# Kernel tuning notes

Hardware: AMD Instinct MI355X
Metric: run time of the kernel (lower is better)

Reference implementation:

```python
import jax, jax.numpy as jnp
import numpy as np

EPS = 1e-5
RES = [12000, 9000, 6000, 4000]
CH = [9, 64, 128, 256]
SKIPS = 3
FC_N = 128


def batchnorm(x, g, b):
    # train-mode BatchNorm2d over (batch, face) dims; x: [B, C, F]
    m = x.mean(axis=(0, 2), keepdims=True)
    v = x.var(axis=(0, 2), keepdims=True)
    xn = (x - m) * jax.lax.rsqrt(v + EPS)
    return xn * g[None, :, None] + b[None, :, None]


def mesh_conv(x, nbr, w):
    # x: [B, C, F]; nbr: [F, 3] neighbor face ids; w: [O, C, 4]
    n = x[:, :, nbr]                      # [B, C, F, 3] irregular gather
    n1, n2, n3 = n[..., 0], n[..., 1], n[..., 2]
    G = jnp.stack([
        x,
        n1 + n2 + n3,
        jnp.abs(n1 - n2) + jnp.abs(n2 - n3) + jnp.abs(n3 - n1),
        jnp.maximum(jnp.maximum(n1, n2), n3),
    ], axis=-1)                           # [B, C, F, 4] symmetric features
    return jnp.einsum('ocj,bcfj->bof', w, G)


def mres_conv(x, nbr, wc, ws, bng, bnb):
    # MResConvFace: conv0 -> skips x (bn(relu) -> conv) -> +skip -> relu
    x = mesh_conv(x, nbr, wc)
    x1 = x
    for i in range(SKIPS):
        x = batchnorm(jax.nn.relu(x), bng[i], bnb[i])
        x = mesh_conv(x, nbr, ws[i])
    return jax.nn.relu(x + x1)


def setup_inputs() -> dict:
    key = jax.random.key(0)
    ks = jax.random.split(key, 64)
    it = iter(range(64))
    d = {}
    d['x'] = jax.random.normal(ks[next(it)], (8, CH[0], RES[0]), dtype=jnp.float32)
    for i in range(3):
        d[f'nbr{i}'] = jax.random.randint(ks[next(it)], (RES[i], 3), 0, RES[i], dtype=jnp.int32)
        d[f'pool{i}'] = jax.random.randint(ks[next(it)], (RES[i + 1], 3), 0, RES[i], dtype=jnp.int32)
    for i in range(3):
        cin, cout = CH[i], CH[i + 1]
        d[f'wc{i}'] = jax.random.normal(ks[next(it)], (cout, cin, 4), dtype=jnp.float32) * (1.0 / np.sqrt(4 * cin))
        d[f'ws{i}'] = jax.random.normal(ks[next(it)], (SKIPS, cout, cout, 4), dtype=jnp.float32) * (1.0 / np.sqrt(4 * cout))
        d[f'bng{i}'] = jnp.ones((SKIPS, cout), dtype=jnp.float32)
        d[f'bnb{i}'] = jnp.zeros((SKIPS, cout), dtype=jnp.float32)
        d[f'ng{i}'] = jnp.ones((cout,), dtype=jnp.float32)
        d[f'nb{i}'] = jnp.zeros((cout,), dtype=jnp.float32)
    d['fc1_w'] = jax.random.normal(ks[next(it)], (FC_N, CH[-1]), dtype=jnp.float32) * (1.0 / np.sqrt(CH[-1]))
    d['fc1_b'] = jnp.zeros((FC_N,), dtype=jnp.float32)
    d['fc2_w'] = jax.random.normal(ks[next(it)], (1, FC_N), dtype=jnp.float32) * (1.0 / np.sqrt(FC_N))
    d['fc2_b'] = jnp.zeros((1,), dtype=jnp.float32)
    return d


def reference(x, nbr0, nbr1, nbr2, pool0, pool1, pool2,
              wc0, ws0, bng0, bnb0, ng0, nb0,
              wc1, ws1, bng1, bnb1, ng1, nb1,
              wc2, ws2, bng2, bnb2, ng2, nb2,
              fc1_w, fc1_b, fc2_w, fc2_b):
    nbrs = [nbr0, nbr1, nbr2]
    pools = [pool0, pool1, pool2]
    wcs, wss = [wc0, wc1, wc2], [ws0, ws1, ws2]
    bngs, bnbs = [bng0, bng1, bng2], [bnb0, bnb1, bnb2]
    ngs, nbs = [ng0, ng1, ng2], [nb0, nb1, nb2]
    for i in range(3):
        x = mres_conv(x, nbrs[i], wcs[i], wss[i], bngs[i], bnbs[i])
        x = jax.nn.relu(batchnorm(x, ngs[i], nbs[i]))
        x = x[:, :, pools[i]].mean(axis=-1)   # MeshPoolFace: collapse 3 faces -> 1
    x = x.mean(axis=-1)                        # global AvgPool1d over faces -> [B, C]
    h = jax.nn.relu(x @ fc1_w.T + fc1_b)
    return jax.nn.sigmoid(h @ fc2_w.T + fc2_b)  # [B, 1]
```

## Files before the change

### kernel.cpp

```cpp
#include <hip/hip_runtime.h>
#include <math.h>

#define NPART 64
#define TILE_F 16

typedef unsigned short u16;
typedef __attribute__((ext_vector_type(8))) short short8;
typedef __attribute__((ext_vector_type(4))) float f32x4;

__device__ __forceinline__ float relu_(float v){ return fmaxf(v, 0.f); }

__device__ __forceinline__ u16 f2bf(float x){
  unsigned u = __float_as_uint(x);
  u = (u + 0x7fffu + ((u >> 16) & 1u)) >> 16;
  return (u16)u;
}

static __device__ __forceinline__ f32x4 mfma_bf16(short8 a, short8 b, f32x4 c){
  asm("v_mfma_f32_16x16x32_bf16 %0, %1, %2, %0" : "+v"(c) : "v"(a), "v"(b));
  return c;
}

template<int CIN,int COUT,int WR,int NWR,bool BN,bool STATS,bool RES>
__global__ __launch_bounds__(NWR*(COUT/64)*64) void mconv_kernel(
    const float* __restrict__ xin, const int* __restrict__ nbr,
    const u16* __restrict__ wbf,
    const float* __restrict__ ps_in, const float* __restrict__ gamma,
    const float* __restrict__ beta, const float* __restrict__ res,
    float* __restrict__ out, float* __restrict__ psum,
    int F, float invN)
{
  constexpr int nWc = COUT/64;
  constexpr int T   = NWR*nWc*64;
  constexpr int BR  = NWR*WR;
  constexpr int K   = 4*CIN;
  constexpr int NSTEP = CIN/16;
  constexpr int ITEMS = (BR*4)/T;
  constexpr int NRF   = WR/16;

  __shared__ __align__(16) u16 Gs[2][BR*64];
  __shared__ float ls[STATS?COUT:1], lq[STATS?COUT:1];
  __shared__ float aS[BN?CIN:1], dS[BN?CIN:1];

  const int t=threadIdx.x, lane=t&63, wid=t>>6;
  const int wm=wid/nWc, wc=wid%nWc;
  const int l15=lane&15, kq=lane>>4;

  if (BN){
    for (int c=t;c<CIN;c+=T){
      float s=0.f,q=0.f;
      #pragma unroll 4
      for (int p=0;p<NPART;p++){ s+=ps_in[p*256+c]; q+=ps_in[(NPART+p)*256+c]; }
      float m=s*invN, v=q*invN-m*m;
      float ai=gamma[c]*rsqrtf(v+1e-5f);
      aS[c]=ai; dS[c]=beta[c]-m*ai;
    }
  }
  if (STATS){ for (int i=t;i<COUT;i+=T){ ls[i]=0.f; lq[i]=0.f; } }
  __syncthreads();

  const float *P0[ITEMS],*P1[ITEMS],*P2[ITEMS],*P3[ITEMS];
  #pragma unroll
  for (int i=0;i<ITEMS;i++){
    int idx=i*T+t, gr=idx>>2, c4q=idx&3;
    int rg=blockIdx.x*BR+gr;
    int b=rg/F, f=rg-b*F;
    int i1=nbr[f*3+0], i2=nbr[f*3+1], i3=nbr[f*3+2];
    const float* xb=xin+(size_t)b*F*CIN+c4q*4;
    P0[i]=xb+(size_t)f *CIN; P1[i]=xb+(size_t)i1*CIN;
    P2[i]=xb+(size_t)i2*CIN; P3[i]=xb+(size_t)i3*CIN;
  }

  const u16* wp = wbf + (size_t)(wc*64+l15)*K + kq*8;
  auto BLD=[&](int cg,int j)->short8{
    return *(const short8*)(wp + (size_t)cg*16*K + (size_t)j*32);
  };
  auto ADS=[&](int pb,int rr,int h)->short8{
    int r=wm*WR+rr*16+l15;
    int sl=h*4+kq;
    return *(const short8*)&Gs[pb][(size_t)r*64 + (size_t)((sl^(r&7))*8)];
  };
  auto GLD=[&](int s,float4 (&g)[ITEMS][4]){
    #pragma unroll
    for (int i=0;i<ITEMS;i++){
      g[i][0]=*(const float4*)(P0[i]+s*16);
      g[i][1]=*(const float4*)(P1[i]+s*16);
      g[i][2]=*(const float4*)(P2[i]+s*16);
      g[i][3]=*(const float4*)(P3[i]+s*16);
    }
  };
  auto BLDW=[&](int pb,int s,float4 (&g)[ITEMS][4]){
    #pragma unroll
    for (int i=0;i<ITEMS;i++){
      int idx=i*T+t, gr=idx>>2, c4q=idx&3;
      float4 S=g[i][0],N1=g[i][1],N2=g[i][2],N3=g[i][3];
      if (BN){
        float4 a4=*(const float4*)&aS[s*16+c4q*4];
        float4 d4=*(const float4*)&dS[s*16+c4q*4];
        S.x =fmaf(relu_(S.x ),a4.x,d4.x); S.y =fmaf(relu_(S.y ),a4.y,d4.y);
        S.z =fmaf(relu_(S.z ),a4.z,d4.z); S.w =fmaf(relu_(S.w ),a4.w,d4.w);
        N1.x=fmaf(relu_(N1.x),a4.x,d4.x); N1.y=fmaf(relu_(N1.y),a4.y,d4.y);
        N1.z=fmaf(relu_(N1.z),a4.z,d4.z); N1.w=fmaf(relu_(N1.w),a4.w,d4.w);
        N2.x=fmaf(relu_(N2.x),a4.x,d4.x); N2.y=fmaf(relu_(N2.y),a4.y,d4.y);
        N2.z=fmaf(relu_(N2.z),a4.z,d4.z); N2.w=fmaf(relu_(N2.w),a4.w,d4.w);
        N3.x=fmaf(relu_(N3.x),a4.x,d4.x); N3.y=fmaf(relu_(N3.y),a4.y,d4.y);
        N3.z=fmaf(relu_(N3.z),a4.z,d4.z); N3.w=fmaf(relu_(N3.w),a4.w,d4.w);
      }
      short8 lo,hi;
      #define FEAT(dst,i0,sv,av,bv,cv) \
        dst[i0+0]=(short)f2bf(sv); \
        dst[i0+1]=(short)f2bf(av+bv+cv); \
        dst[i0+2]=(short)f2bf(fabsf(av-bv)+fabsf(bv-cv)+fabsf(cv-av)); \
        dst[i0+3]=(short)f2bf(fmaxf(fmaxf(av,bv),cv));
      FEAT(lo,0,S.x,N1.x,N2.x,N3.x)
      FEAT(lo,4,S.y,N1.y,N2.y,N3.y)
      FEAT(hi,0,S.z,N1.z,N2.z,N3.z)
      FEAT(hi,4,S.w,N1.w,N2.w,N3.w)
      #undef FEAT
      u16* rowp=&Gs[pb][(size_t)gr*64];
      *(short8*)&rowp[(size_t)(((2*c4q  )^(gr&7))*8)]=lo;
      *(short8*)&rowp[(size_t)(((2*c4q+1)^(gr&7))*8)]=hi;
    }
  };

  f32x4 acc[NRF][4];
  #pragma unroll
  for (int rr=0;rr<NRF;rr++)
    #pragma unroll
    for (int cg=0;cg<4;cg++){ f32x4 z={0.f,0.f,0.f,0.f}; acc[rr][cg]=z; }

  short8 B0[4],B1[4];
  #pragma unroll
  for (int cg=0;cg<4;cg++) B0[cg]=BLD(cg,0);
  #pragma unroll
  for (int cg=0;cg<4;cg++) B1[cg]=BLD(cg,1);

  auto MSTEP=[&](int pb,int s){
    short8 A[NRF];
    #pragma unroll
    for (int rr=0;rr<NRF;rr++) A[rr]=ADS(pb,rr,0);
    #pragma unroll
    for (int rr=0;rr<NRF;rr++)
      #pragma unroll
      for (int cg=0;cg<4;cg++) acc[rr][cg]=mfma_bf16(A[rr],B0[cg],acc[rr][cg]);
    if (s+1<NSTEP){
      #pragma unroll
      for (int cg=0;cg<4;cg++) B0[cg]=BLD(cg,2*(s+1));
    }
    #pragma unroll
    for (int rr=0;rr<NRF;rr++) A[rr]=ADS(pb,rr,1);
    #pragma unroll
    for (int rr=0;rr<NRF;rr++)
      #pragma unroll
      for (int cg=0;cg<4;cg++) acc[rr][cg]=mfma_bf16(A[rr],B1[cg],acc[rr][cg]);
    if (s+1<NSTEP){
      #pragma unroll
      for (int cg=0;cg<4;cg++) B1[cg]=BLD(cg,2*(s+1)+1);
    }
  };

  float4 gA[ITEMS][4], gB[ITEMS][4];
  GLD(0,gA); BLDW(0,0,gA);
  GLD(1,gA);
  __syncthreads();

  for (int s=0;s<NSTEP;s+=2){
    if (s+2<NSTEP) GLD(s+2,gB);
    MSTEP(0,s);
    if (s+1<NSTEP) BLDW(1,s+1,gA);
    __syncthreads();
    if (s+3<NSTEP) GLD(s+3,gA);
    if (s+1<NSTEP) MSTEP(1,s+1);
    if (s+2<NSTEP) BLDW(0,s+2,gB);
    __syncthreads();
  }

  #pragma unroll
  for (int cg=0;cg<4;cg++){
    const int col=wc*64+cg*16+l15;
    float rs=0.f,rq=0.f;
    #pragma unroll
    for (int rr=0;rr<NRF;rr++){
      const size_t rbase=(size_t)blockIdx.x*BR + wm*WR + rr*16 + kq*4;
      #pragma unroll
      for (int q=0;q<4;q++){
        size_t idx=(rbase+q)*COUT+col;
        float v=acc[rr][cg][q];
        if (RES){ v += res[idx]; v = relu_(v); }
        out[idx]=v;
        if (STATS){ float rv = RES ? v : relu_(v); rs+=rv; rq+=rv*rv; }
      }
    }
    if (STATS){ atomicAdd(&ls[col],rs); atomicAdd(&lq[col],rq); }
  }
  if (STATS){
    __syncthreads();
    const int part=blockIdx.x&(NPART-1);
    for (int i=t;i<COUT;i+=T){
      atomicAdd(&psum[(size_t)part*256+i],ls[i]);
      atomicAdd(&psum[(size_t)(NPART+part)*256+i],lq[i]);
    }
  }
}

template<int CIN,int COUT,bool BN,bool STATS>
__global__ __launch_bounds__(256) void conv_kernel(
    const float* __restrict__ xin, const int* __restrict__ nbr,
    const float* __restrict__ Wt, const float* __restrict__ bn_a,
    const float* __restrict__ bn_d,
    float* __restrict__ out, float* __restrict__ psum, int F)
{
  constexpr int K = 4*CIN;
  constexpr int ROWLEN = K + 4;
  __shared__ float Gs[TILE_F][ROWLEN];
  __shared__ int   nI[TILE_F*3];
  __shared__ float ls[STATS?COUT:1];
  __shared__ float lq[STATS?COUT:1];
  const int t = threadIdx.x;
  const int fbase = blockIdx.x*TILE_F;
  const int b = blockIdx.y;
  const float* __restrict__ xb = xin + (size_t)b*F*CIN;

  if (t < TILE_F*3){ int fi=t/3, j=t-fi*3; int fg=fbase+fi; nI[t]=(fg<F)?nbr[fg*3+j]:0; }
  if (STATS){ for (int i=t;i<COUT;i+=256){ ls[i]=0.f; lq[i]=0.f; } }
  __syncthreads();

  for (int idx=t; idx<TILE_F*CIN; idx+=256){
    int fi=idx/CIN, c=idx-fi*CIN;
    int fg=fbase+fi;
    float* dst=&Gs[fi][4*c];
    if (fg<F){
      int i1=nI[fi*3], i2=nI[fi*3+1], i3=nI[fi*3+2];
      float s =xb[(size_t)fg*CIN+c];
      float v1=xb[(size_t)i1*CIN+c];
      float v2=xb[(size_t)i2*CIN+c];
      float v3=xb[(size_t)i3*CIN+c];
      if (BN){ float a=bn_a[c], dd=bn_d[c];
        s=fmaf(relu_(s),a,dd); v1=fmaf(relu_(v1),a,dd);
        v2=fmaf(relu_(v2),a,dd); v3=fmaf(relu_(v3),a,dd); }
      dst[0]=s; dst[1]=v1+v2+v3;
      dst[2]=fabsf(v1-v2)+fabsf(v2-v3)+fabsf(v3-v1);
      dst[3]=fmaxf(fmaxf(v1,v2),v3);
    } else { dst[0]=0.f;dst[1]=0.f;dst[2]=0.f;dst[3]=0.f; }
  }
  __syncthreads();

  constexpr int OQ=COUT/4;
  constexpr int R=256/OQ;
  constexpr int FPT=TILE_F/R;
  const int col=t%OQ, row=t/OQ;
  const int o0=col*4, f0=row*FPT;
  float4 acc[FPT];
  #pragma unroll
  for (int fi=0;fi<FPT;fi++){ acc[fi].x=0.f;acc[fi].y=0.f;acc[fi].z=0.f;acc[fi].w=0.f; }

  for (int k=0;k<K;k+=4){
    float4 w0=*(const float4*)&Wt[(size_t)(k+0)*COUT+o0];
    float4 w1=*(const float4*)&Wt[(size_t)(k+1)*COUT+o0];
    float4 w2=*(const float4*)&Wt[(size_t)(k+2)*COUT+o0];
    float4 w3=*(const float4*)&Wt[(size_t)(k+3)*COUT+o0];
    #pragma unroll
    for (int fi=0;fi<FPT;fi++){
      float4 g=*(const float4*)&Gs[f0+fi][k];
      acc[fi].x=fmaf(g.x,w0.x,fmaf(g.y,w1.x,fmaf(g.z,w2.x,fmaf(g.w,w3.x,acc[fi].x))));
      acc[fi].y=fmaf(g.x,w0.y,fmaf(g.y,w1.y,fmaf(g.z,w2.y,fmaf(g.w,w3.y,acc[fi].y))));
      acc[fi].z=fmaf(g.x,w0.z,fmaf(g.y,w1.z,fmaf(g.z,w2.z,fmaf(g.w,w3.z,acc[fi].z))));
      acc[fi].w=fmaf(g.x,w0.w,fmaf(g.y,w1.w,fmaf(g.z,w2.w,fmaf(g.w,w3.w,acc[fi].w))));
    }
  }

  float4 rs={0,0,0,0}, rq={0,0,0,0};
  #pragma unroll
  for (int fi=0;fi<FPT;fi++){
    int fg=fbase+f0+fi;
    if (fg<F){
      *(float4*)&out[((size_t)b*F+fg)*COUT+o0]=acc[fi];
      if (STATS){
        float rx=relu_(acc[fi].x), ry=relu_(acc[fi].y);
        float rz=relu_(acc[fi].z), rw=relu_(acc[fi].w);
        rs.x+=rx; rs.y+=ry; rs.z+=rz; rs.w+=rw;
        rq.x+=rx*rx; rq.y+=ry*ry; rq.z+=rz*rz; rq.w+=rw*rw;
      }
    }
  }
  if (STATS){
    atomicAdd(&ls[o0+0],rs.x); atomicAdd(&ls[o0+1],rs.y);
    atomicAdd(&ls[o0+2],rs.z); atomicAdd(&ls[o0+3],rs.w);
    atomicAdd(&lq[o0+0],rq.x); atomicAdd(&lq[o0+1],rq.y);
    atomicAdd(&lq[o0+2],rq.z); atomicAdd(&lq[o0+3],rq.w);
    __syncthreads();
    int part=(blockIdx.y*gridDim.x+blockIdx.x)&(NPART-1);
    for (int i=t;i<COUT;i+=256){
      atomicAdd(&psum[(size_t)part*256+i], ls[i]);
      atomicAdd(&psum[(size_t)(NPART+part)*256+i], lq[i]);
    }
  }
}

__global__ __launch_bounds__(256) void pool_kernel(
    const float* __restrict__ z, const int* __restrict__ pl,
    const float* __restrict__ ps_in, const float* __restrict__ gamma,
    const float* __restrict__ beta,
    float* __restrict__ out, int C4, int F, int Fn, int n4, float invN)
{
  __shared__ float aS[256], dS[256];
  const int C=C4*4;
  const int t=threadIdx.x;
  if (t<C){
    float s=0.f,q=0.f;
    #pragma unroll 4
    for (int p=0;p<NPART;p++){ s+=ps_in[p*256+t]; q+=ps_in[(NPART+p)*256+t]; }
    float m=s*invN, v=q*invN-m*m;
    float ai=gamma[t]*rsqrtf(v+1e-5f);
    aS[t]=ai; dS[t]=beta[t]-m*ai;
  }
  __syncthreads();
  for (int i=blockIdx.x*256+t; i<n4; i+=gridDim.x*256){
    int c4=i%C4; int rest=i/C4; int p=rest%Fn; int b=rest/Fn;
    int p0=pl[p*3], p1=pl[p*3+1], p2=pl[p*3+2];
    float4 a4=*(const float4*)&aS[4*c4], d4=*(const float4*)&dS[4*c4];
    float4 v0=*(const float4*)&z[((size_t)b*F+p0)*C+4*c4];
    float4 v1=*(const float4*)&z[((size_t)b*F+p1)*C+4*c4];
    float4 v2=*(const float4*)&z[((size_t)b*F+p2)*C+4*c4];
    float4 r;
    r.x=(relu_(fmaf(v0.x,a4.x,d4.x))+relu_(fmaf(v1.x,a4.x,d4.x))+relu_(fmaf(v2.x,a4.x,d4.x)))*(1.f/3.f);
    r.y=(relu_(fmaf(v0.y,a4.y,d4.y))+relu_(fmaf(v1.y,a4.y,d4.y))+relu_(fmaf(v2.y,a4.y,d4.y)))*(1.f/3.f);
    r.z=(relu_(fmaf(v0.z,a4.z,d4.z))+relu_(fmaf(v1.z,a4.z,d4.z))+relu_(fmaf(v2.z,a4.z,d4.z)))*(1.f/3.f);
    r.w=(relu_(fmaf(v0.w,a4.w,d4.w))+relu_(fmaf(v1.w,a4.w,d4.w))+relu_(fmaf(v2.w,a4.w,d4.w)))*(1.f/3.f);
    *(float4*)&out[((size_t)b*Fn+p)*C+4*c4]=r;
  }
}

__global__ __launch_bounds__(256) void colsum_kernel(
    const float* __restrict__ x, float* __restrict__ bc, int F, int chunk)
{
  int b=blockIdx.y; int f0=blockIdx.x*chunk;
  int c=threadIdx.x;
  int fe=f0+chunk; if (fe>F) fe=F;
  float s=0.f;
  for (int f=f0;f<fe;f++) s+=x[((size_t)b*F+f)*256+c];
  atomicAdd(&bc[b*256+c], s);
}

__global__ __launch_bounds__(256) void head_kernel(
    const float* __restrict__ bc, const float* __restrict__ w1,
    const float* __restrict__ b1, const float* __restrict__ w2,
    const float* __restrict__ b2, float* __restrict__ outp, float invF)
{
  __shared__ float xm[8*256];
  __shared__ float h[8*128];
  int t=threadIdx.x;
  for (int i=t;i<2048;i+=256) xm[i]=bc[i]*invF;
  __syncthreads();
  #pragma unroll
  for (int r=0;r<4;r++){
    int idx=t+r*256; int b=idx>>7, j=idx&127;
    float s=b1[j];
    for (int c=0;c<256;c++) s=fmaf(xm[b*256+c],w1[j*256+c],s);
    h[idx]=relu_(s);
  }
  __syncthreads();
  if (t<8){
    float s=b2[0];
    for (int j=0;j<128;j++) s=fmaf(h[t*128+j],w2[j],s);
    outp[t]=1.f/(1.f+expf(-s));
  }
}

__global__ __launch_bounds__(256) void transpose_in_kernel(
    const float* __restrict__ x, float* __restrict__ xt, int F)
{
  int i=blockIdx.x*256+threadIdx.x;
  int total=8*9*F;
  if (i<total){ int f=i%F; int c=(i/F)%9; int b=i/(9*F);
    xt[((size_t)b*F+f)*9+c]=x[i]; }
}

__global__ __launch_bounds__(256) void transpose_w_kernel(
    const float* __restrict__ w, float* __restrict__ wt, int K, int COUT)
{
  int i=blockIdx.x*256+threadIdx.x;
  if (i<K*COUT){ int o=i/K, k=i-o*K; wt[(size_t)k*COUT+o]=w[i]; }
}

__global__ __launch_bounds__(256) void cvt_bf16_kernel(
    const float* __restrict__ w, u16* __restrict__ o, int n)
{
  int i=blockIdx.x*256+threadIdx.x;
  if (i<n) o[i]=f2bf(w[i]);
}


template<int CIN,int COUT,int WR,int NWR,bool BN,bool STATS,bool RES>
static void launch_mconv(const float* xin, const int* nbr, const u16* wbf,
                         const float* ps_in, const float* gamma, const float* beta,
                         const float* res, float* out, float* ps_out,
                         int F, float invN, hipStream_t stream)
{
  constexpr int T  = NWR*(COUT/64)*64;
  constexpr int BR = NWR*WR;
  int M = 8*F;
  mconv_kernel<CIN,COUT,WR,NWR,BN,STATS,RES><<<M/BR, T, 0, stream>>>(
      xin,nbr,wbf,ps_in,gamma,beta,res,out,ps_out,F,invN);
}

extern "C" void kernel_launch(void* const* d_in, const int* in_sizes, int n_in,
                              void* d_out, int out_size, void* d_ws, size_t ws_size,
                              hipStream_t stream)
{
  const float* x    =(const float*)d_in[0];
  const int*  nbr0  =(const int*)d_in[1];
  const int*  pool0 =(const int*)d_in[2];
  const int*  nbr1  =(const int*)d_in[3];
  const int*  pool1 =(const int*)d_in[4];
  const int*  nbr2  =(const int*)d_in[5];
  const int*  pool2 =(const int*)d_in[6];
  const float* wc0  =(const float*)d_in[7];
  const float* ws0  =(const float*)d_in[8];
  const float* bng0 =(const float*)d_in[9];
  const float* bnb0 =(const float*)d_in[10];
  const float* ng0  =(const float*)d_in[11];
  const float* nb0  =(const float*)d_in[12];
  const float* wc1  =(const float*)d_in[13];
  const float* ws1  =(const float*)d_in[14];
  const float* bng1 =(const float*)d_in[15];
  const float* bnb1 =(const float*)d_in[16];
  const float* ng1  =(const float*)d_in[17];
  const float* nb1  =(const float*)d_in[18];
  const float* wc2  =(const float*)d_in[19];
  const float* ws2  =(const float*)d_in[20];
  const float* bng2 =(const float*)d_in[21];
  const float* bnb2 =(const float*)d_in[22];
  const float* ng2  =(const float*)d_in[23];
  const float* nb2  =(const float*)d_in[24];
  const float* fc1w =(const float*)d_in[25];
  const float* fc1b =(const float*)d_in[26];
  const float* fc2w =(const float*)d_in[27];
  const float* fc2b =(const float*)d_in[28];
  float* outp=(float*)d_out;

  char* base=(char*)d_ws;
  size_t off=0;
  auto alloc=[&](size_t nbytes)->void*{
    void* p=base+off; off=(off+nbytes+255)&~(size_t)255; return p; };

  float* psum0 =(float*)alloc((size_t)12*131072);
  float* bc    =(float*)alloc(8192);
  float* wt_wc0=(float*)alloc((size_t)36*64*4);
  u16*   bws0  =(u16*)alloc((size_t)3*16384*2);
  u16*   bwc1  =(u16*)alloc((size_t)32768*2);
  u16*   bws1  =(u16*)alloc((size_t)3*65536*2);
  u16*   bwc2  =(u16*)alloc((size_t)131072*2);
  u16*   bws2  =(u16*)alloc((size_t)3*262144*2);
  float* xT    =(float*)alloc((size_t)8*12000*9*4);
  float* B0    =(float*)alloc((size_t)49152000);
  float* B1    =(float*)alloc((size_t)49152000);
  float* B2    =(float*)alloc((size_t)49152000);
  if (off>ws_size) return;

  auto PS=[&](int i){ return psum0+(size_t)i*32768; };

  hipMemsetAsync(psum0,0,(size_t)12*131072+8192,stream);

  { int n=8*9*12000; transpose_in_kernel<<<(n+255)/256,256,0,stream>>>(x,xT,12000); }
  { int n=36*64; transpose_w_kernel<<<(n+255)/256,256,0,stream>>>(wc0,wt_wc0,36,64); }
  auto cv=[&](const float* w,u16* o,int n){
    cvt_bf16_kernel<<<(n+255)/256,256,0,stream>>>(w,o,n); };
  cv(ws0,bws0,3*16384);
  cv(wc1,bwc1,32768);
  cv(ws1,bws1,3*65536);
  cv(wc2,bwc2,131072);
  cv(ws2,bws2,3*262144);

  {
    const int F=12000; const float invN=1.f/(8.f*F);
    dim3 grid((F+TILE_F-1)/TILE_F, 8);
    conv_kernel<9,64,false,true><<<grid,256,0,stream>>>(xT,nbr0,wt_wc0,nullptr,nullptr,B0,PS(0),F);
    launch_mconv<64,64,32,2,true,true ,false>(B0,nbr0,bws0,        PS(0),bng0,     bnb0,     nullptr,B1,PS(1),F,invN,stream);
    launch_mconv<64,64,32,2,true,true ,false>(B1,nbr0,bws0+16384,  PS(1),bng0+64,  bnb0+64,  nullptr,B2,PS(2),F,invN,stream);
    launch_mconv<64,64,32,2,true,true ,true >(B2,nbr0,bws0+32768,  PS(2),bng0+128, bnb0+128, B0,     B1,PS(3),F,invN,stream);
    int n4p=8*9000*16; int gp=(n4p+255)/256; if (gp>2048) gp=2048;
    pool_kernel<<<gp,256,0,stream>>>(B1,pool0,PS(3),ng0,nb0,B2,16,F,9000,n4p,invN);
  }
  {
    const int F=9000; const float invN=1.f/(8.f*F);
    launch_mconv<64,128,64,1,false,true ,false>(B2,nbr1,bwc1,         nullptr,nullptr,  nullptr,  nullptr,B0,PS(4),F,invN,stream);
    launch_mconv<128,128,64,1,true,true ,false>(B0,nbr1,bws1,         PS(4),bng1,      bnb1,     nullptr,B1,PS(5),F,invN,stream);
    launch_mconv<128,128,64,1,true,true ,false>(B1,nbr1,bws1+65536,   PS(5),bng1+128,  bnb1+128, nullptr,B2,PS(6),F,invN,stream);
    launch_mconv<128,128,64,1,true,true ,true >(B2,nbr1,bws1+131072,  PS(6),bng1+256,  bnb1+256, B0,     B1,PS(7),F,invN,stream);
    int n4p=8*6000*32; int gp=(n4p+255)/256; if (gp>2048) gp=2048;
    pool_kernel<<<gp,256,0,stream>>>(B1,pool1,PS(7),ng1,nb1,B0,32,F,6000,n4p,invN);
  }
  {
    const int F=6000; const float invN=1.f/(8.f*F);
    launch_mconv<128,256,64,1,false,true ,false>(B0,nbr2,bwc2,         nullptr,nullptr,  nullptr,  nullptr,B1,PS(8),F,invN,stream);
    launch_mconv<256,256,64,1,true,true ,false>(B1,nbr2,bws2,         PS(8), bng2,     bnb2,     nullptr,B2,PS(9),F,invN,stream);
    launch_mconv<256,256,64,1,true,true ,false>(B2,nbr2,bws2+262144,  PS(9), bng2+256, bnb2+256, nullptr,B0,PS(10),F,invN,stream);
    launch_mconv<256,256,64,1,true,true ,true >(B0,nbr2,bws2+524288,  PS(10),bng2+512, bnb2+512, B1,     B2,PS(11),F,invN,stream);
    int n4p=8*4000*64; int gp=(n4p+255)/256; if (gp>2048) gp=2048;
    pool_kernel<<<gp,256,0,stream>>>(B2,pool2,PS(11),ng2,nb2,B0,64,F,4000,n4p,invN);
    colsum_kernel<<<dim3(16,8),256,0,stream>>>(B0,bc,4000,250);
  }
  head_kernel<<<1,256,0,stream>>>(bc,fc1w,fc1b,fc2w,fc2b,outp,1.f/4000.f);
}
```

Baseline: 965.9 us.

## Interleave batches across blocks and simplify pipeline to single-stage prefetch loop

Remaps block indices so consecutive blocks cover the same face tile across the 8 batches, with per-batch tiles padded and bounds-checked so that F need not divide evenly. This is meant to improve cache reuse of the neighbor indices and shared gathered rows across batches. The double-register-buffer, two-step unrolled software pipeline is replaced by a single loop that prefetches the next step into one register set. That cuts register pressure but may overlap global loads with the MFMAs less well. It also adds bounds-check overhead and some wasted work in the padded tail tiles.

```diff
diff --git a/kernel.cpp b/kernel.cpp
--- a/kernel.cpp
+++ b/kernel.cpp
@@ -46,6 +46,9 @@
   const int wm=wid/nWc, wc=wid%nWc;
   const int l15=lane&15, kq=lane>>4;
 
+  const int batch = blockIdx.x & 7;
+  const int row0  = (blockIdx.x >> 3) * BR;
+
   if (BN){
     for (int c=t;c<CIN;c+=T){
       float s=0.f,q=0.f;
@@ -63,10 +66,10 @@
   #pragma unroll
   for (int i=0;i<ITEMS;i++){
     int idx=i*T+t, gr=idx>>2, c4q=idx&3;
-    int rg=blockIdx.x*BR+gr;
-    int b=rg/F, f=rg-b*F;
+    int f=row0+gr;
+    if (f>=F) f=F-1;
     int i1=nbr[f*3+0], i2=nbr[f*3+1], i3=nbr[f*3+2];
-    const float* xb=xin+(size_t)b*F*CIN+c4q*4;
+    const float* xb=xin+(size_t)batch*F*CIN+c4q*4;
     P0[i]=xb+(size_t)f *CIN; P1[i]=xb+(size_t)i1*CIN;
     P2[i]=xb+(size_t)i2*CIN; P3[i]=xb+(size_t)i3*CIN;
   }
@@ -135,7 +138,14 @@
   #pragma unroll
   for (int cg=0;cg<4;cg++) B1[cg]=BLD(cg,1);
 
-  auto MSTEP=[&](int pb,int s){
+  { float4 g0[ITEMS][4]; GLD(0,g0); BLDW(0,0,g0); }
+  __syncthreads();
+
+  #pragma unroll 2
+  for (int s=0;s<NSTEP;s++){
+    const int pb=s&1;
+    float4 g[ITEMS][4];
+    if (s+1<NSTEP) GLD(s+1,g);
     short8 A[NRF];
     #pragma unroll
     for (int rr=0;rr<NRF;rr++) A[rr]=ADS(pb,rr,0);
@@ -156,39 +166,29 @@
     if (s+1<NSTEP){
       #pragma unroll
       for (int cg=0;cg<4;cg++) B1[cg]=BLD(cg,2*(s+1)+1);
-    }
-  };
-
-  float4 gA[ITEMS][4], gB[ITEMS][4];
-  GLD(0,gA); BLDW(0,0,gA);
-  GLD(1,gA);
-  __syncthreads();
-
-  for (int s=0;s<NSTEP;s+=2){
-    if (s+2<NSTEP) GLD(s+2,gB);
-    MSTEP(0,s);
-    if (s+1<NSTEP) BLDW(1,s+1,gA);
+      BLDW(pb^1,s+1,g);
+    }
     __syncthreads();
-    if (s+3<NSTEP) GLD(s+3,gA);
-    if (s+1<NSTEP) MSTEP(1,s+1);
-    if (s+2<NSTEP) BLDW(0,s+2,gB);
-    __syncthreads();
-  }
-
+  }
+
+  const size_t bbase=(size_t)batch*F;
   #pragma unroll
   for (int cg=0;cg<4;cg++){
     const int col=wc*64+cg*16+l15;
     float rs=0.f,rq=0.f;
     #pragma unroll
     for (int rr=0;rr<NRF;rr++){
-      const size_t rbase=(size_t)blockIdx.x*BR + wm*WR + rr*16 + kq*4;
+      const int r0=row0 + wm*WR + rr*16 + kq*4;
       #pragma unroll
       for (int q=0;q<4;q++){
-        size_t idx=(rbase+q)*COUT+col;
-        float v=acc[rr][cg][q];
-        if (RES){ v += res[idx]; v = relu_(v); }
-        out[idx]=v;
-        if (STATS){ float rv = RES ? v : relu_(v); rs+=rv; rq+=rv*rv; }
+        int r=r0+q;
+        if (r<F){
+          size_t idx=(bbase+r)*COUT+col;
+          float v=acc[rr][cg][q];
+          if (RES){ v += res[idx]; v = relu_(v); }
+          out[idx]=v;
+          if (STATS){ float rv = RES ? v : relu_(v); rs+=rv; rq+=rv*rv; }
+        }
       }
     }
     if (STATS){ atomicAdd(&ls[col],rs); atomicAdd(&lq[col],rq); }
@@ -399,8 +399,8 @@
 {
   constexpr int T  = NWR*(COUT/64)*64;
   constexpr int BR = NWR*WR;
-  int M = 8*F;
-  mconv_kernel<CIN,COUT,WR,NWR,BN,STATS,RES><<<M/BR, T, 0, stream>>>(
+  int nb = (F + BR - 1)/BR;
+  mconv_kernel<CIN,COUT,WR,NWR,BN,STATS,RES><<<8*nb, T, 0, stream>>>(
       xin,nbr,wbf,ps_in,gamma,beta,res,out,ps_out,F,invN);
 }
 
```

Result: faster. 918.4 us (-4.9%).
